# Kernel tuning notes

Measured on AMD Instinct MI355X. Metric: run time of the kernel, lower is better.

## Reference

```python
import jax, jax.numpy as jnp
import numpy as np

NUM_HEADS = 16
MAX_FREQ = 10.0
LN_EPS = 1e-5
PI = float(np.pi)


def layer_norm(x, w, b):
    mu = jnp.mean(x, axis=-1, keepdims=True)
    var = jnp.mean(jnp.square(x - mu), axis=-1, keepdims=True)
    return (x - mu) * jax.lax.rsqrt(var + LN_EPS) * w + b


def rotate_half(x):
    # interleaved pairs: (x0,x1,x2,x3,...) -> (-x1,x0,-x3,x2,...)
    x1 = x[..., 0::2]
    x2 = x[..., 1::2]
    return jnp.stack((-x2, x1), axis=-1).reshape(x.shape)


def drofe(q, k, freqband, demo):
    # q, k: [B,H,N,D]; freqband: [N,2] (lower/upper band bound); demo: [B,2] (age, gender)
    D = q.shape[-1]
    freqs = jnp.linspace(1.0, MAX_FREQ / 2.0, D // 4).astype(q.dtype) * PI  # [D/4]
    ang = jnp.concatenate([freqband[:, 0:1] * freqs, freqband[:, 1:2] * freqs], axis=-1)  # [N, D/2]
    ang = jnp.repeat(ang, 2, axis=-1)  # [N, D]
    cos, sin = jnp.cos(ang), jnp.sin(ang)
    age = demo[:, 0][:, None, None, None]
    gender = demo[:, 1][:, None, None, None]
    q = q * cos * age + rotate_half(q) * sin * gender
    k = k * cos * age + rotate_half(k) * sin * gender
    return q, k


def setup_inputs() -> dict:
    key = jax.random.key(0)
    ks = jax.random.split(key, 16)
    B, N, C, F = 8, 1024, 1024, 4096
    s = 0.02
    return {
        "x": jax.random.normal(ks[0], (B, N, C), jnp.float32),
        "demographic_info": jax.random.uniform(ks[1], (B, 2), jnp.float32),
        "explanation": jax.random.normal(ks[2], (B, N, C), jnp.float32),
        "freqband": jax.random.uniform(ks[3], (N, 2), jnp.float32) * 50.0,
        "w_qkv": jax.random.normal(ks[4], (C, 3 * C), jnp.float32) * s,
        "w_proj": jax.random.normal(ks[5], (C, C), jnp.float32) * s,
        "b_proj": jnp.zeros((C,), jnp.float32),
        "gamma1": jnp.full((C,), 1e-5, jnp.float32),
        "gamma2": jnp.full((C,), 1e-5, jnp.float32),
        "ln1_w": jnp.ones((C,), jnp.float32),
        "ln1_b": jnp.zeros((C,), jnp.float32),
        "ln2_w": jnp.ones((C,), jnp.float32),
        "ln2_b": jnp.zeros((C,), jnp.float32),
        "w1": jax.random.normal(ks[6], (C, F), jnp.float32) * s,
        "b1": jnp.zeros((F,), jnp.float32),
        "w2": jax.random.normal(ks[7], (F, C), jnp.float32) * s,
        "b2": jnp.zeros((C,), jnp.float32),
    }


def reference(x, demographic_info, explanation, freqband, w_qkv, w_proj, b_proj,
              gamma1, gamma2, ln1_w, ln1_b, ln2_w, ln2_b, w1, b1, w2, b2):
    B, N, C = x.shape
    H = NUM_HEADS
    D = C // H

    def split_qkv(t):
        return (t @ w_qkv).reshape(B, N, 3, H, D).transpose(2, 0, 3, 1, 4)  # [3,B,H,N,D]

    v = split_qkv(x)[2]
    qkv_e = split_qkv(explanation)  # explanation-swap: q,k come from explanation
    q, k = qkv_e[0], qkv_e[1]
    q, k = drofe(q, k, freqband, demographic_info)

    attn = jax.nn.softmax(jnp.einsum('bhnd,bhmd->bhnm', q, k) * (D ** -0.5), axis=-1)
    o = jnp.einsum('bhnm,bhmd->bhnd', attn, v).transpose(0, 2, 1, 3).reshape(B, N, C)
    o = o @ w_proj + b_proj

    x = layer_norm(x + gamma1 * o, ln1_w, ln1_b)  # post-norm + LayerScale
    h = jax.nn.gelu(x @ w1 + b1, approximate=False) @ w2 + b2
    x = layer_norm(x + gamma2 * h, ln2_w, ln2_b)
    return x
```

## Files before the change

kernel.cpp:

```cpp
#include <hip/hip_runtime.h>
#include <hip/hip_bf16.h>
#include <math.h>

typedef __attribute__((ext_vector_type(8))) short bf16x8;
typedef __attribute__((ext_vector_type(8))) unsigned short u16x8;
typedef __attribute__((ext_vector_type(4))) float f32x4;
typedef __attribute__((ext_vector_type(4))) unsigned short u16x4;

__device__ inline unsigned short f2bf(float f) {
    union { float f; unsigned u; } v; v.f = f;
    unsigned r = (v.u + 0x7fff + ((v.u >> 16) & 1)) >> 16;
    return (unsigned short)r;
}
__device__ inline float bf2f(unsigned short u) {
    union { unsigned u; float f; } v; v.u = ((unsigned)u) << 16; return v.f;
}

#define GLL16(gp, lp) __builtin_amdgcn_global_load_lds(                      \
    (const __attribute__((address_space(1))) void*)(gp),                     \
    (__attribute__((address_space(3))) void*)(lp), 16, 0, 0)

template<int EPI, int OUT_BF, int BK>
__global__ __launch_bounds__(256, 4) void gemm97o(
    const unsigned short* __restrict__ A,
    const unsigned short* __restrict__ Bt,
    const float* __restrict__ bias,
    void* __restrict__ Cout,
    int M, int Nn, int K, int ldc)
{
    constexpr int SPR = BK / 8;
    constexpr int RB  = BK * 2;
    __shared__ unsigned char lds[256 * BK * 2];
    const int tid = threadIdx.x;
    const int w = tid >> 6, lane = tid & 63;
    const int lk = lane & 15, lg = lane >> 4;
    const int wr = w >> 1, wc = w & 1;
    const int nbn = Nn >> 7;
    const int nb = gridDim.x;
    int bid = blockIdx.x;
    int swz = (nb & 7) ? bid : (bid & 7) * (nb >> 3) + (bid >> 3);
    const int bm = (swz / nbn) << 7, bn = (swz % nbn) << 7;

    f32x4 acc[4][4] = {};

    for (int k0 = 0; k0 < K; k0 += BK) {
        #pragma unroll
        for (int i = 0; i < SPR; ++i) {
            int s = tid + i * 256;
            int r = s / SPR, c = s % SPR;
            int cs;
            if constexpr (SPR == 4) cs = (c ^ r ^ (r >> 2)) & 3;
            else                    cs = c ^ (r & 7);
            const unsigned short* gp = (r < 128)
                ? A  + (size_t)(bm + r) * K + k0 + cs * 8
                : Bt + (size_t)(bn + (r - 128)) * K + k0 + cs * 8;
            GLL16(gp, &lds[s * 16]);
        }
        __syncthreads();

        #pragma unroll
        for (int kk = 0; kk < BK / 32; ++kk) {
            bf16x8 af[4], bfr[4];
            #pragma unroll
            for (int m = 0; m < 4; ++m) {
                int row = wr * 64 + m * 16 + lk;
                int sl;
                if constexpr (SPR == 4) sl = ((kk * 4 + lg) ^ row ^ (row >> 2)) & 3;
                else                    sl = (kk * 4 + lg) ^ (row & 7);
                af[m] = *(const bf16x8*)&lds[row * RB + sl * 16];
            }
            #pragma unroll
            for (int n = 0; n < 4; ++n) {
                int row = wc * 64 + n * 16 + lk;
                int sl;
                if constexpr (SPR == 4) sl = ((kk * 4 + lg) ^ row ^ (row >> 2)) & 3;
                else                    sl = (kk * 4 + lg) ^ (row & 7);
                bfr[n] = *(const bf16x8*)&lds[128 * RB + row * RB + sl * 16];
            }
            #pragma unroll
            for (int m = 0; m < 4; ++m)
                #pragma unroll
                for (int n = 0; n < 4; ++n)
                    acc[m][n] = __builtin_amdgcn_mfma_f32_16x16x32_bf16(af[m], bfr[n], acc[m][n], 0, 0, 0);
        }
        __syncthreads();
    }

    #pragma unroll
    for (int m = 0; m < 4; ++m) {
        int row = bm + wr * 64 + m * 16 + lg * 4;
        #pragma unroll
        for (int n = 0; n < 4; ++n) {
            int col = bn + wc * 64 + n * 16 + lk;
            #pragma unroll
            for (int r = 0; r < 4; ++r) {
                float v = acc[m][n][r];
                if (EPI >= 1) v += bias[col];
                if (EPI == 2) {
                    float u = v * 0.7978845608f * (1.0f + 0.044715f * v * v);
                    v = v / (1.0f + __expf(-2.0f * u));
                }
                if (OUT_BF)
                    ((unsigned short*)Cout)[(size_t)(row + r) * ldc + col] = f2bf(v);
                else
                    ((float*)Cout)[(size_t)(row + r) * ldc + col] = v;
            }
        }
    }
}

__global__ __launch_bounds__(256) void cvt_bf16(
    const float* __restrict__ src, unsigned short* __restrict__ dst, int n)
{
    int i = (blockIdx.x * 256 + threadIdx.x) * 4;
    if (i < n) {
        float4 v = *(const float4*)(src + i);
        u16x4 o = { f2bf(v.x), f2bf(v.y), f2bf(v.z), f2bf(v.w) };
        *(u16x4*)(dst + i) = o;
    }
}

__global__ __launch_bounds__(256) void transpose_cvt(
    const float* __restrict__ src, unsigned short* __restrict__ dst, int R, int Cc)
{
    __shared__ float t[32][33];
    const int bc = blockIdx.x * 32, br = blockIdx.y * 32;
    const int tx = threadIdx.x & 31, ty = threadIdx.x >> 5;
    #pragma unroll
    for (int i = 0; i < 4; ++i)
        t[ty + i * 8][tx] = src[(size_t)(br + ty + i * 8) * Cc + bc + tx];
    __syncthreads();
    #pragma unroll
    for (int i = 0; i < 4; ++i)
        dst[(size_t)(bc + ty + i * 8) * R + br + tx] = f2bf(t[tx][ty + i * 8]);
}

__global__ __launch_bounds__(256) void drofe_bf(
    const unsigned short* __restrict__ QK, unsigned short* __restrict__ Qo,
    unsigned short* __restrict__ Ko,
    const float* __restrict__ freqband, const float* __restrict__ demo, int N)
{
    const float PI_F = 3.14159265358979323846f;
    int idx = blockIdx.x * 256 + threadIdx.x;
    int col2 = idx & 511;
    int row  = idx >> 9;
    int n = row & (N - 1), b = row >> 10;
    int i  = col2 & 31;
    int ii = (i < 16) ? i : i - 16;
    float fb = (i < 16) ? freqband[n * 2 + 0] : freqband[n * 2 + 1];
    float freq = (1.0f + (float)ii * (4.0f / 15.0f)) * PI_F;
    float ang = fb * freq;
    float cv = cosf(ang), sv = sinf(ang);
    float ca = cv * demo[b * 2 + 0];
    float sg = sv * demo[b * 2 + 1];
    const unsigned* qk = (const unsigned*)(QK + (size_t)row * 2048);
    unsigned qu = qk[col2], ku = qk[512 + col2];
    float qe = bf2f((unsigned short)qu), qo_ = bf2f((unsigned short)(qu >> 16));
    float ke = bf2f((unsigned short)ku), ko_ = bf2f((unsigned short)(ku >> 16));
    const float s8 = 0.125f;
    unsigned qres = (unsigned)f2bf((qe * ca - qo_ * sg) * s8)
                  | ((unsigned)f2bf((qo_ * ca + qe * sg) * s8) << 16);
    unsigned kres = (unsigned)f2bf(ke * ca - ko_ * sg)
                  | ((unsigned)f2bf(ko_ * ca + ke * sg) << 16);
    ((unsigned*)Qo)[(size_t)row * 512 + col2] = qres;
    ((unsigned*)Ko)[(size_t)row * 512 + col2] = kres;
}

__global__ __launch_bounds__(256) void attn_mfma(
    const unsigned short* __restrict__ Q, const unsigned short* __restrict__ K,
    const unsigned short* __restrict__ V, unsigned short* __restrict__ O,
    int B, int H, int N)
{
    __shared__ unsigned short Ks[64 * 64];
    __shared__ unsigned short Vt[64 * 72];
    __shared__ unsigned short Ps[4][16 * 72];

    const int bi = blockIdx.x;
    const int bh = (bi & 7) + 8 * ((bi >> 3) & 15);
    const int q0 = (bi >> 7) * 64;
    const int b = bh >> 4, h = bh & 15;
    const int tid = threadIdx.x;
    const int w = tid >> 6, lane = tid & 63;
    const int lg = lane >> 4, lk = lane & 15;

    bf16x8 qf[2];
    {
        const unsigned short* qrow = Q + (size_t)(b * N + q0 + w * 16 + lk) * 1024 + h * 64;
        qf[0] = *(const bf16x8*)(qrow + lg * 8);
        qf[1] = *(const bf16x8*)(qrow + 32 + lg * 8);
    }

    f32x4 o[4] = {};
    float m_run = -INFINITY, l_run = 0.f;

    for (int t0 = 0; t0 < N; t0 += 64) {
        const size_t kvbase = (size_t)(b * N + t0) * 1024 + h * 64;
        #pragma unroll
        for (int it = 0; it < 2; ++it) {
            int s = it * 256 + tid;
            int row = s >> 3, cb = (s & 7) << 4;
            int dby = cb ^ ((row & 7) << 4);
            GLL16(K + kvbase + (size_t)row * 1024 + (dby >> 1), &Ks[s * 8]);
        }
        {
            int c = tid >> 5, k0 = (tid & 31) * 2;
            const unsigned short* vp = V + kvbase + (size_t)k0 * 1024 + c * 8;
            u16x8 va = *(const u16x8*)vp;
            u16x8 vb = *(const u16x8*)(vp + 1024);
            #pragma unroll
            for (int j = 0; j < 8; ++j) {
                unsigned val = (unsigned)va[j] | ((unsigned)vb[j] << 16);
                *(unsigned*)&Vt[(c * 8 + j) * 72 + k0] = val;
            }
        }
        __syncthreads();

        f32x4 s4[4];
        #pragma unroll
        for (int sub = 0; sub < 4; ++sub) {
            f32x4 acc = {0.f, 0.f, 0.f, 0.f};
            #pragma unroll
            for (int kh = 0; kh < 2; ++kh) {
                int cc = (kh * 64 + lg * 16) ^ ((lk & 7) << 4);
                bf16x8 kf = *(const bf16x8*)&Ks[(sub * 16 + lk) * 64 + (cc >> 1)];
                acc = __builtin_amdgcn_mfma_f32_16x16x32_bf16(kf, qf[kh], acc, 0, 0, 0);
            }
            s4[sub] = acc;
        }

        float tm = -INFINITY;
        #pragma unroll
        for (int sub = 0; sub < 4; ++sub)
            #pragma unroll
            for (int r = 0; r < 4; ++r) tm = fmaxf(tm, s4[sub][r]);
        tm = fmaxf(tm, __shfl_xor(tm, 16));
        tm = fmaxf(tm, __shfl_xor(tm, 32));
        float mn = fmaxf(m_run, tm);
        float corr = __expf(m_run - mn);
        m_run = mn;
        float psum = 0.f;
        unsigned pw[4][2];
        #pragma unroll
        for (int sub = 0; sub < 4; ++sub) {
            float p0 = __expf(s4[sub][0] - mn);
            float p1 = __expf(s4[sub][1] - mn);
            float p2 = __expf(s4[sub][2] - mn);
            float p3 = __expf(s4[sub][3] - mn);
            psum += (p0 + p1) + (p2 + p3);
            pw[sub][0] = (__float_as_uint(p0) >> 16) | (__float_as_uint(p1) & 0xffff0000u);
            pw[sub][1] = (__float_as_uint(p2) >> 16) | (__float_as_uint(p3) & 0xffff0000u);
        }
        psum += __shfl_xor(psum, 16);
        psum += __shfl_xor(psum, 32);
        l_run = l_run * corr + psum;
        #pragma unroll
        for (int ds = 0; ds < 4; ++ds)
            #pragma unroll
            for (int r = 0; r < 4; ++r) o[ds][r] *= corr;
        #pragma unroll
        for (int sub = 0; sub < 4; ++sub) {
            *(unsigned*)&Ps[w][lk * 72 + sub * 16 + lg * 4]     = pw[sub][0];
            *(unsigned*)&Ps[w][lk * 72 + sub * 16 + lg * 4 + 2] = pw[sub][1];
        }
        asm volatile("s_waitcnt lgkmcnt(0)" ::: "memory");

        #pragma unroll
        for (int kh = 0; kh < 2; ++kh) {
            bf16x8 pf = *(const bf16x8*)&Ps[w][lk * 72 + kh * 32 + lg * 8];
            #pragma unroll
            for (int ds = 0; ds < 4; ++ds) {
                bf16x8 vf = *(const bf16x8*)&Vt[(ds * 16 + lk) * 72 + kh * 32 + lg * 8];
                o[ds] = __builtin_amdgcn_mfma_f32_16x16x32_bf16(vf, pf, o[ds], 0, 0, 0);
            }
        }
        __syncthreads();
    }

    {
        unsigned short* orow = O + (size_t)(b * N + q0 + w * 16 + lk) * 1024 + h * 64;
        float rinv = 1.0f / l_run;
        #pragma unroll
        for (int ds = 0; ds < 4; ++ds) {
            u16x4 pk = { f2bf(o[ds][0] * rinv), f2bf(o[ds][1] * rinv),
                         f2bf(o[ds][2] * rinv), f2bf(o[ds][3] * rinv) };
            *(u16x4*)(orow + ds * 16 + lg * 4) = pk;
        }
    }
}

__global__ __launch_bounds__(256) void ln_res_kernel(
    const float* __restrict__ x, const unsigned short* __restrict__ y,
    const float* __restrict__ gamma, const float* __restrict__ w,
    const float* __restrict__ bia, float* __restrict__ out,
    unsigned short* __restrict__ out_bf, int C)
{
    const int row = blockIdx.x;
    __shared__ float buf[1024];
    __shared__ float red[8];
    const size_t base = (size_t)row * C;
    float s = 0.f, ss = 0.f;
    for (int c = threadIdx.x; c < C; c += 256) {
        float v = x[base + c] + gamma[c] * bf2f(y[base + c]);
        buf[c] = v; s += v; ss += v * v;
    }
    #pragma unroll
    for (int msk = 1; msk < 64; msk <<= 1) { s += __shfl_xor(s, msk); ss += __shfl_xor(ss, msk); }
    int wv = threadIdx.x >> 6, lane = threadIdx.x & 63;
    if (lane == 0) { red[wv * 2] = s; red[wv * 2 + 1] = ss; }
    __syncthreads();
    if (threadIdx.x == 0) {
        float S = 0.f, SS = 0.f;
        #pragma unroll
        for (int i = 0; i < 4; ++i) { S += red[2 * i]; SS += red[2 * i + 1]; }
        red[0] = S; red[1] = SS;
    }
    __syncthreads();
    float mu = red[0] / C;
    float var = red[1] / C - mu * mu;
    float rstd = rsqrtf(var + 1e-5f);
    for (int c = threadIdx.x; c < C; c += 256) {
        float v = (buf[c] - mu) * rstd * w[c] + bia[c];
        out[base + c] = v;
        if (out_bf) out_bf[base + c] = f2bf(v);
    }
}

extern "C" void kernel_launch(void* const* d_in, const int* in_sizes, int n_in,
                              void* d_out, int out_size, void* d_ws, size_t ws_size,
                              hipStream_t stream)
{
    const float* x      = (const float*)d_in[0];
    const float* demo   = (const float*)d_in[1];
    const float* expl   = (const float*)d_in[2];
    const float* fb     = (const float*)d_in[3];
    const float* w_qkv  = (const float*)d_in[4];
    const float* w_proj = (const float*)d_in[5];
    const float* b_proj = (const float*)d_in[6];
    const float* gamma1 = (const float*)d_in[7];
    const float* gamma2 = (const float*)d_in[8];
    const float* ln1_w  = (const float*)d_in[9];
    const float* ln1_b  = (const float*)d_in[10];
    const float* ln2_w  = (const float*)d_in[11];
    const float* ln2_b  = (const float*)d_in[12];
    const float* w1     = (const float*)d_in[13];
    const float* b1     = (const float*)d_in[14];
    const float* w2     = (const float*)d_in[15];
    const float* b2     = (const float*)d_in[16];
    float* out = (float*)d_out;

    const int B = 8, N = 1024, C = 1024, F = 4096, H = 16;
    const int M = B * N;
    const size_t Mi = 1048576;

    float* ws = (float*)d_ws;
    unsigned short* QKbf = (unsigned short*)ws;
    unsigned short* Obf  = (unsigned short*)ws;
    unsigned short* H2   = (unsigned short*)ws;
    unsigned short* Qbf  = (unsigned short*)(ws + 8 * Mi);
    unsigned short* Kbf  = (unsigned short*)(ws + 12 * Mi);
    unsigned short* Vbf  = (unsigned short*)(ws + 16 * Mi);
    unsigned short* Hid  = (unsigned short*)(ws + 8 * Mi);
    unsigned short* Ebf  = (unsigned short*)(ws + 24 * Mi);
    unsigned short* Xbf  = (unsigned short*)(ws + 28 * Mi);
    unsigned short* Pb   = (unsigned short*)(ws + 24 * Mi);
    float*          X1   = ws + 32 * Mi;
    unsigned short* X1bf = (unsigned short*)(ws + 40 * Mi);
    unsigned short* Wt   = (unsigned short*)(ws + 44 * Mi);
    unsigned short* wqkvT  = Wt;
    unsigned short* wprojT = Wt + (size_t)3145728;
    unsigned short* w1T    = wprojT + (size_t)1048576;
    unsigned short* w2T    = w1T + (size_t)4194304;

    dim3 blk(256);
    const int MC = M * C;

    hipLaunchKernelGGL(cvt_bf16, dim3(MC / 1024), blk, 0, stream, expl, Ebf, MC);
    hipLaunchKernelGGL(cvt_bf16, dim3(MC / 1024), blk, 0, stream, x, Xbf, MC);
    hipLaunchKernelGGL(transpose_cvt, dim3(96, 32), blk, 0, stream, w_qkv, wqkvT, C, 3 * C);
    hipLaunchKernelGGL(transpose_cvt, dim3(32, 32), blk, 0, stream, w_proj, wprojT, C, C);
    hipLaunchKernelGGL(transpose_cvt, dim3(128, 32), blk, 0, stream, w1, w1T, C, F);
    hipLaunchKernelGGL(transpose_cvt, dim3(32, 128), blk, 0, stream, w2, w2T, F, C);

    hipLaunchKernelGGL((gemm97o<0,1,32>), dim3(64 * 16), blk, 0, stream, Ebf, wqkvT, (const float*)nullptr, (void*)QKbf, M, 2048, C, 2048);
    hipLaunchKernelGGL((gemm97o<0,1,32>), dim3(64 * 8), blk, 0, stream, Xbf, wqkvT + (size_t)2048 * 1024, (const float*)nullptr, (void*)Vbf, M, 1024, C, 1024);

    hipLaunchKernelGGL(drofe_bf, dim3(M * 512 / 256), blk, 0, stream, QKbf, Qbf, Kbf, fb, demo, N);

    hipLaunchKernelGGL(attn_mfma, dim3(B * H * (N / 64)), blk, 0, stream, Qbf, Kbf, Vbf, Obf, B, H, N);

    hipLaunchKernelGGL((gemm97o<1,1,32>), dim3(64 * 8), blk, 0, stream, Obf, wprojT, b_proj, (void*)Pb, M, 1024, C, 1024);

    hipLaunchKernelGGL(ln_res_kernel, dim3(M), blk, 0, stream, x, Pb, gamma1, ln1_w, ln1_b, X1, X1bf, C);

    hipLaunchKernelGGL((gemm97o<2,1,32>), dim3(64 * 32), blk, 0, stream, X1bf, w1T, b1, (void*)Hid, M, F, C, F);
    hipLaunchKernelGGL((gemm97o<1,1,64>), dim3(64 * 8), blk, 0, stream, Hid, w2T, b2, (void*)H2, M, 1024, F, 1024);

    hipLaunchKernelGGL(ln_res_kernel, dim3(M), blk, 0, stream, X1, H2, gamma2, ln2_w, ln2_b, out, (unsigned short*)nullptr, C);
}
```

Before: 426.4 us.

## Double-buffer GEMM LDS tiles and add lazy softmax rescale with MFMA priority

The GEMM kernel now keeps two LDS buffers and issues the global-to-LDS loads for the next K tile before computing the current one. This needs only one barrier per iteration and is meant to overlap memory latency with MFMA work; the K=4096 GEMM moves from BK=64 to BK=32. The attention kernel skips the running-max rescale of the output accumulators unless the new max exceeds the old one by more than 8 (FA4-style lazy rescaling), and raises wave priority around MFMA sections. The lazy rescale lets exponentials grow up to e^8 before renormalizing, which could affect precision when P is packed to bf16.

```diff
diff --git a/kernel.cpp b/kernel.cpp
--- a/kernel.cpp
+++ b/kernel.cpp
@@ -20,17 +20,15 @@
     (const __attribute__((address_space(1))) void*)(gp),                     \
     (__attribute__((address_space(3))) void*)(lp), 16, 0, 0)
 
-template<int EPI, int OUT_BF, int BK>
-__global__ __launch_bounds__(256, 4) void gemm97o(
+template<int EPI, int OUT_BF>
+__global__ __launch_bounds__(256, 4) void gemm2ph128(
     const unsigned short* __restrict__ A,
     const unsigned short* __restrict__ Bt,
     const float* __restrict__ bias,
     void* __restrict__ Cout,
     int M, int Nn, int K, int ldc)
 {
-    constexpr int SPR = BK / 8;
-    constexpr int RB  = BK * 2;
-    __shared__ unsigned char lds[256 * BK * 2];
+    __shared__ unsigned char lds[2][16384];
     const int tid = threadIdx.x;
     const int w = tid >> 6, lane = tid & 63;
     const int lk = lane & 15, lg = lane >> 4;
@@ -43,47 +41,45 @@
 
     f32x4 acc[4][4] = {};
 
-    for (int k0 = 0; k0 < K; k0 += BK) {
-        #pragma unroll
-        for (int i = 0; i < SPR; ++i) {
+    auto stage = [&](int buf, int k0) {
+        #pragma unroll
+        for (int i = 0; i < 4; ++i) {
             int s = tid + i * 256;
-            int r = s / SPR, c = s % SPR;
-            int cs;
-            if constexpr (SPR == 4) cs = (c ^ r ^ (r >> 2)) & 3;
-            else                    cs = c ^ (r & 7);
+            int r = s >> 2, c = s & 3;
+            int cs = (c ^ r ^ (r >> 2)) & 3;
             const unsigned short* gp = (r < 128)
                 ? A  + (size_t)(bm + r) * K + k0 + cs * 8
                 : Bt + (size_t)(bn + (r - 128)) * K + k0 + cs * 8;
-            GLL16(gp, &lds[s * 16]);
-        }
+            GLL16(gp, &lds[buf][s * 16]);
+        }
+    };
+
+    const int NT = K >> 5;
+    stage(0, 0);
+    __syncthreads();
+    int cur = 0;
+    for (int t = 0; t < NT; ++t) {
+        if (t + 1 < NT) stage(cur ^ 1, (t + 1) << 5);
+        bf16x8 af[4], bfr[4];
+        #pragma unroll
+        for (int m = 0; m < 4; ++m) {
+            int row = wr * 64 + m * 16 + lk;
+            int sl = (lg ^ row ^ (row >> 2)) & 3;
+            af[m] = *(const bf16x8*)&lds[cur][row * 64 + sl * 16];
+        }
+        #pragma unroll
+        for (int n = 0; n < 4; ++n) {
+            int row = wc * 64 + n * 16 + lk;
+            int sl = (lg ^ row ^ (row >> 2)) & 3;
+            bfr[n] = *(const bf16x8*)&lds[cur][8192 + row * 64 + sl * 16];
+        }
+        #pragma unroll
+        for (int m = 0; m < 4; ++m)
+            #pragma unroll
+            for (int n = 0; n < 4; ++n)
+                acc[m][n] = __builtin_amdgcn_mfma_f32_16x16x32_bf16(af[m], bfr[n], acc[m][n], 0, 0, 0);
         __syncthreads();
-
-        #pragma unroll
-        for (int kk = 0; kk < BK / 32; ++kk) {
-            bf16x8 af[4], bfr[4];
-            #pragma unroll
-            for (int m = 0; m < 4; ++m) {
-                int row = wr * 64 + m * 16 + lk;
-                int sl;
-                if constexpr (SPR == 4) sl = ((kk * 4 + lg) ^ row ^ (row >> 2)) & 3;
-                else                    sl = (kk * 4 + lg) ^ (row & 7);
-                af[m] = *(const bf16x8*)&lds[row * RB + sl * 16];
-            }
-            #pragma unroll
-            for (int n = 0; n < 4; ++n) {
-                int row = wc * 64 + n * 16 + lk;
-                int sl;
-                if constexpr (SPR == 4) sl = ((kk * 4 + lg) ^ row ^ (row >> 2)) & 3;
-                else                    sl = (kk * 4 + lg) ^ (row & 7);
-                bfr[n] = *(const bf16x8*)&lds[128 * RB + row * RB + sl * 16];
-            }
-            #pragma unroll
-            for (int m = 0; m < 4; ++m)
-                #pragma unroll
-                for (int n = 0; n < 4; ++n)
-                    acc[m][n] = __builtin_amdgcn_mfma_f32_16x16x32_bf16(af[m], bfr[n], acc[m][n], 0, 0, 0);
-        }
-        __syncthreads();
+        cur ^= 1;
     }
 
     #pragma unroll
@@ -216,6 +212,7 @@
         __syncthreads();
 
         f32x4 s4[4];
+        __builtin_amdgcn_s_setprio(1);
         #pragma unroll
         for (int sub = 0; sub < 4; ++sub) {
             f32x4 acc = {0.f, 0.f, 0.f, 0.f};
@@ -227,36 +224,42 @@
             }
             s4[sub] = acc;
         }
-
-        float tm = -INFINITY;
+        __builtin_amdgcn_s_setprio(0);
+
+        float pmax = -INFINITY;
         #pragma unroll
         for (int sub = 0; sub < 4; ++sub)
             #pragma unroll
-            for (int r = 0; r < 4; ++r) tm = fmaxf(tm, s4[sub][r]);
-        tm = fmaxf(tm, __shfl_xor(tm, 16));
-        tm = fmaxf(tm, __shfl_xor(tm, 32));
-        float mn = fmaxf(m_run, tm);
-        float corr = __expf(m_run - mn);
-        m_run = mn;
+            for (int r = 0; r < 4; ++r) pmax = fmaxf(pmax, s4[sub][r]);
+        pmax = fmaxf(pmax, __shfl_xor(pmax, 16));
+        pmax = fmaxf(pmax, __shfl_xor(pmax, 32));
+
+        if (!__all(pmax - m_run <= 8.0f)) {
+            float mn = fmaxf(m_run, pmax);
+            float corr = __expf(m_run - mn);
+            m_run = mn;
+            l_run *= corr;
+            #pragma unroll
+            for (int ds = 0; ds < 4; ++ds)
+                #pragma unroll
+                for (int r = 0; r < 4; ++r) o[ds][r] *= corr;
+        }
+
         float psum = 0.f;
         unsigned pw[4][2];
         #pragma unroll
         for (int sub = 0; sub < 4; ++sub) {
-            float p0 = __expf(s4[sub][0] - mn);
-            float p1 = __expf(s4[sub][1] - mn);
-            float p2 = __expf(s4[sub][2] - mn);
-            float p3 = __expf(s4[sub][3] - mn);
+            float p0 = __expf(s4[sub][0] - m_run);
+            float p1 = __expf(s4[sub][1] - m_run);
+            float p2 = __expf(s4[sub][2] - m_run);
+            float p3 = __expf(s4[sub][3] - m_run);
             psum += (p0 + p1) + (p2 + p3);
             pw[sub][0] = (__float_as_uint(p0) >> 16) | (__float_as_uint(p1) & 0xffff0000u);
             pw[sub][1] = (__float_as_uint(p2) >> 16) | (__float_as_uint(p3) & 0xffff0000u);
         }
         psum += __shfl_xor(psum, 16);
         psum += __shfl_xor(psum, 32);
-        l_run = l_run * corr + psum;
-        #pragma unroll
-        for (int ds = 0; ds < 4; ++ds)
-            #pragma unroll
-            for (int r = 0; r < 4; ++r) o[ds][r] *= corr;
+        l_run += psum;
         #pragma unroll
         for (int sub = 0; sub < 4; ++sub) {
             *(unsigned*)&Ps[w][lk * 72 + sub * 16 + lg * 4]     = pw[sub][0];
@@ -264,6 +267,7 @@
         }
         asm volatile("s_waitcnt lgkmcnt(0)" ::: "memory");
 
+        __builtin_amdgcn_s_setprio(1);
         #pragma unroll
         for (int kh = 0; kh < 2; ++kh) {
             bf16x8 pf = *(const bf16x8*)&Ps[w][lk * 72 + kh * 32 + lg * 8];
@@ -273,6 +277,7 @@
                 o[ds] = __builtin_amdgcn_mfma_f32_16x16x32_bf16(vf, pf, o[ds], 0, 0, 0);
             }
         }
+        __builtin_amdgcn_s_setprio(0);
         __syncthreads();
     }
 
@@ -381,19 +386,19 @@
     hipLaunchKernelGGL(transpose_cvt, dim3(128, 32), blk, 0, stream, w1, w1T, C, F);
     hipLaunchKernelGGL(transpose_cvt, dim3(32, 128), blk, 0, stream, w2, w2T, F, C);
 
-    hipLaunchKernelGGL((gemm97o<0,1,32>), dim3(64 * 16), blk, 0, stream, Ebf, wqkvT, (const float*)nullptr, (void*)QKbf, M, 2048, C, 2048);
-    hipLaunchKernelGGL((gemm97o<0,1,32>), dim3(64 * 8), blk, 0, stream, Xbf, wqkvT + (size_t)2048 * 1024, (const float*)nullptr, (void*)Vbf, M, 1024, C, 1024);
+    hipLaunchKernelGGL((gemm2ph128<0,1>), dim3(64 * 16), blk, 0, stream, Ebf, wqkvT, (const float*)nullptr, (void*)QKbf, M, 2048, C, 2048);
+    hipLaunchKernelGGL((gemm2ph128<0,1>), dim3(64 * 8), blk, 0, stream, Xbf, wqkvT + (size_t)2048 * 1024, (const float*)nullptr, (void*)Vbf, M, 1024, C, 1024);
 
     hipLaunchKernelGGL(drofe_bf, dim3(M * 512 / 256), blk, 0, stream, QKbf, Qbf, Kbf, fb, demo, N);
 
     hipLaunchKernelGGL(attn_mfma, dim3(B * H * (N / 64)), blk, 0, stream, Qbf, Kbf, Vbf, Obf, B, H, N);
 
-    hipLaunchKernelGGL((gemm97o<1,1,32>), dim3(64 * 8), blk, 0, stream, Obf, wprojT, b_proj, (void*)Pb, M, 1024, C, 1024);
+    hipLaunchKernelGGL((gemm2ph128<1,1>), dim3(64 * 8), blk, 0, stream, Obf, wprojT, b_proj, (void*)Pb, M, 1024, C, 1024);
 
     hipLaunchKernelGGL(ln_res_kernel, dim3(M), blk, 0, stream, x, Pb, gamma1, ln1_w, ln1_b, X1, X1bf, C);
 
-    hipLaunchKernelGGL((gemm97o<2,1,32>), dim3(64 * 32), blk, 0, stream, X1bf, w1T, b1, (void*)Hid, M, F, C, F);
-    hipLaunchKernelGGL((gemm97o<1,1,64>), dim3(64 * 8), blk, 0, stream, Hid, w2T, b2, (void*)H2, M, 1024, F, 1024);
+    hipLaunchKernelGGL((gemm2ph128<2,1>), dim3(64 * 32), blk, 0, stream, X1bf, w1T, b1, (void*)Hid, M, F, C, F);
+    hipLaunchKernelGGL((gemm2ph128<1,1>), dim3(64 * 8), blk, 0, stream, Hid, w2T, b2, (void*)H2, M, 1024, F, 1024);
 
     hipLaunchKernelGGL(ln_res_kernel, dim3(M), blk, 0, stream, X1, H2, gamma2, ln2_w, ln2_b, out, (unsigned short*)nullptr, C);
 }
```

New measurement: 426.9 us. Within noise of the previous version (+0.1%).
